# Performance work log

Hardware: AMD Instinct MI355X
Metric: run time of the kernel (lower is better)

## Reference

```python
import jax, jax.numpy as jnp
import numpy as np

B, S, DM = 2, 2048, 1024
H, KVH = 16, 4
DK = DM // H          # 64
KV_DIM = DK * KVH     # 256
REP = H // KVH        # 4


def setup_inputs() -> dict:
    key = jax.random.key(0)
    ks = jax.random.split(key, 8)
    return {
        "query": jax.random.normal(ks[0], (B, S, DM), jnp.float32),
        "key": jax.random.normal(ks[1], (B, S, DM), jnp.float32),
        "value": jax.random.normal(ks[2], (B, S, DM), jnp.float32),
        "Wq": jax.random.normal(ks[3], (DM, DM), jnp.float32) * 0.02,
        "bq": jnp.zeros((DM,), jnp.float32),
        "Wk": jax.random.normal(ks[4], (KV_DIM, DM), jnp.float32) * 0.02,
        "bk": jnp.zeros((KV_DIM,), jnp.float32),
        "Wv": jax.random.normal(ks[5], (KV_DIM, DM), jnp.float32) * 0.02,
        "bv": jnp.zeros((KV_DIM,), jnp.float32),
        "Wo": jax.random.normal(ks[6], (DM, DM), jnp.float32) * 0.02,
        "bo": jnp.zeros((DM,), jnp.float32),
    }


def reference(query, key, value, Wq, bq, Wk, bk, Wv, bv, Wo, bo):
    b, s, dm = query.shape
    # torch Linear: y = x @ W.T + b
    Q = (query @ Wq.T + bq).reshape(b, s, H, DK).transpose(0, 2, 1, 3)    # [b,H,s,dk]
    K = (key @ Wk.T + bk).reshape(b, s, KVH, DK).transpose(0, 2, 1, 3)    # [b,KVH,s,dk]
    V = (value @ Wv.T + bv).reshape(b, s, KVH, DK).transpose(0, 2, 1, 3)  # [b,KVH,s,dk]
    # group query heads by kv head instead of repeat_interleave-ing K/V
    Qg = Q.reshape(b, KVH, REP, s, DK)                                    # [b,g,r,s,dk]
    scale = 1.0 / np.sqrt(DK)
    scores = jnp.einsum('bgrqd,bgkd->bgrqk', Qg, K) * scale               # [b,g,r,s,s]
    attn = jax.nn.softmax(scores, axis=-1)
    ctx = jnp.einsum('bgrqk,bgkd->bgrqd', attn, V)                        # [b,g,r,s,dk]
    ctx = ctx.reshape(b, H, s, DK).transpose(0, 2, 1, 3).reshape(b, s, dm)
    out = ctx @ Wo.T + bo
    return out, attn.reshape(b, H, s, s)
```

## Files before the change

### kernel.cpp

```cpp
#include <hip/hip_runtime.h>

#define S_LEN 2048
#define DMODEL 1024
#define NH 16
#define NKVH 4
#define DKH 64
#define KVD 256
#define SCALE_LOG2E 0.18033688f

typedef __bf16 bf16;
typedef bf16  bf16x8 __attribute__((ext_vector_type(8)));
typedef bf16  bf16x4 __attribute__((ext_vector_type(4)));
typedef float f32x4  __attribute__((ext_vector_type(4)));
typedef bf16x8 bf16x8_a __attribute__((may_alias));
typedef bf16x4 bf16x4_a __attribute__((may_alias));
typedef float f32x4g __attribute__((ext_vector_type(4), may_alias));

#define VWAIT(N)                                             \
    do {                                                     \
        asm volatile("s_waitcnt vmcnt(" #N ")" ::: "memory");\
        __builtin_amdgcn_sched_barrier(0);                   \
    } while (0)

__device__ __forceinline__ void gll16(const bf16* g, bf16* l) {
    __builtin_amdgcn_global_load_lds(
        (const __attribute__((address_space(1))) void*)g,
        (__attribute__((address_space(3))) void*)l, 16, 0, 0);
}

__global__ __launch_bounds__(256) void cast3_bf16(const float* __restrict__ a,
                                                  const float* __restrict__ b,
                                                  const float* __restrict__ c,
                                                  bf16* __restrict__ oa, bf16* __restrict__ ob,
                                                  bf16* __restrict__ oc, int n4) {
    const float* src = blockIdx.y == 0 ? a : blockIdx.y == 1 ? b : c;
    bf16* dst = blockIdx.y == 0 ? oa : blockIdx.y == 1 ? ob : oc;
    int stride = gridDim.x * blockDim.x;
    for (int i = blockIdx.x * blockDim.x + threadIdx.x; i < n4; i += stride) {
        f32x4g v = ((const f32x4g*)src)[i];
        bf16x4 o;
        o[0] = (bf16)v[0]; o[1] = (bf16)v[1]; o[2] = (bf16)v[2]; o[3] = (bf16)v[3];
        ((bf16x4*)dst)[i] = o;
    }
}

__global__ __launch_bounds__(256) void cast4_bf16(const float* __restrict__ a,
                                                  const float* __restrict__ b,
                                                  const float* __restrict__ c,
                                                  const float* __restrict__ d,
                                                  bf16* __restrict__ oa, bf16* __restrict__ ob,
                                                  bf16* __restrict__ oc, bf16* __restrict__ od,
                                                  int n4big, int n4small) {
    const int y = blockIdx.y;
    const float* src = y == 0 ? a : y == 1 ? b : y == 2 ? c : d;
    bf16* dst = y == 0 ? oa : y == 1 ? ob : y == 2 ? oc : od;
    const int n4 = y < 2 ? n4big : n4small;
    int stride = gridDim.x * blockDim.x;
    for (int i = blockIdx.x * blockDim.x + threadIdx.x; i < n4; i += stride) {
        f32x4g v = ((const f32x4g*)src)[i];
        bf16x4 o;
        o[0] = (bf16)v[0]; o[1] = (bf16)v[1]; o[2] = (bf16)v[2]; o[3] = (bf16)v[3];
        ((bf16x4*)dst)[i] = o;
    }
}

template <int OUTF32>
__device__ __forceinline__ void gemm_body(const bf16* __restrict__ A,
                                          const bf16* __restrict__ Bw,
                                          const float* __restrict__ bias,
                                          void* __restrict__ Cout, int bm, int bn, int N,
                                          int K, bf16* As, bf16* Bs) {
    const int tid = threadIdx.x, wave = tid >> 6, lane = tid & 63;
    const int l15 = lane & 15, lhi = lane >> 4;
    const int wr = (wave >> 1) * 64, wc = (wave & 1) * 64;
    f32x4 acc[4][4] = {};
    const size_t arow0 = (size_t)bm * 128 * K;
    const size_t brow0 = (size_t)bn * 128 * K;

    for (int kt = 0; kt < K; kt += 32) {
#pragma unroll
        for (int i = 0; i < 2; ++i) {
            int base = i * 2048 + wave * 512;
            int flat = base + lane * 8;
            int r = flat >> 5, c = flat & 31;
            gll16(A + arow0 + (size_t)r * K + kt + c, &As[base]);
            gll16(Bw + brow0 + (size_t)r * K + kt + c, &Bs[base]);
        }
        __syncthreads();
        bf16x8 af[4], bfr[4];
#pragma unroll
        for (int mi = 0; mi < 4; ++mi)
            af[mi] = *(const bf16x8_a*)&As[(wr + mi * 16 + l15) * 32 + lhi * 8];
#pragma unroll
        for (int ni = 0; ni < 4; ++ni)
            bfr[ni] = *(const bf16x8_a*)&Bs[(wc + ni * 16 + l15) * 32 + lhi * 8];
#pragma unroll
        for (int mi = 0; mi < 4; ++mi)
#pragma unroll
            for (int ni = 0; ni < 4; ++ni)
                acc[mi][ni] = __builtin_amdgcn_mfma_f32_16x16x32_bf16(
                    af[mi], bfr[ni], acc[mi][ni], 0, 0, 0);
        __syncthreads();
    }
#pragma unroll
    for (int mi = 0; mi < 4; ++mi)
#pragma unroll
        for (int ni = 0; ni < 4; ++ni)
#pragma unroll
            for (int j = 0; j < 4; ++j) {
                int row = bm * 128 + wr + mi * 16 + lhi * 4 + j;
                int col = bn * 128 + wc + ni * 16 + l15;
                float v = acc[mi][ni][j] + bias[col];
                if (OUTF32)
                    ((float*)Cout)[(size_t)row * N + col] = v;
                else
                    ((bf16*)Cout)[(size_t)row * N + col] = (bf16)v;
            }
}

template <int OUTF32>
__global__ __launch_bounds__(256) void gemm_bt(const bf16* __restrict__ A,
                                               const bf16* __restrict__ Bw,
                                               const float* __restrict__ bias,
                                               void* __restrict__ Cout,
                                               int M, int N, int K) {
    __shared__ bf16 As[4096];
    __shared__ bf16 Bs[4096];
    gemm_body<OUTF32>(A, Bw, bias, Cout, blockIdx.x, blockIdx.y, N, K, As, Bs);
}

__global__ __launch_bounds__(256) void gemm_qkv(const bf16* __restrict__ qx,
                                                const bf16* __restrict__ kx,
                                                const bf16* __restrict__ vx,
                                                const bf16* __restrict__ wqx,
                                                const bf16* __restrict__ wkx,
                                                const bf16* __restrict__ wvx,
                                                const float* __restrict__ bq,
                                                const float* __restrict__ bk,
                                                const float* __restrict__ bv,
                                                bf16* __restrict__ Qp, bf16* __restrict__ Kp,
                                                bf16* __restrict__ Vp) {
    __shared__ bf16 As[4096];
    __shared__ bf16 Bs[4096];
    const int by = blockIdx.y;
    const bf16* A;
    const bf16* Bw;
    const float* bias;
    bf16* C;
    int N, bn;
    if (by < 8) {
        A = qx; Bw = wqx; bias = bq; C = Qp; N = 1024; bn = by;
    } else if (by < 10) {
        A = kx; Bw = wkx; bias = bk; C = Kp; N = 256; bn = by - 8;
    } else {
        A = vx; Bw = wvx; bias = bv; C = Vp; N = 256; bn = by - 10;
    }
    gemm_body<0>(A, Bw, bias, C, blockIdx.x, bn, N, 1024, As, Bs);
}

__global__ __launch_bounds__(256) void vtrans(const bf16* __restrict__ V,
                                              bf16* __restrict__ VT) {
    __shared__ bf16 t[64][65];
    const int s0 = blockIdx.x * 64;
    const int bg = blockIdx.y;
    const int b = bg >> 2, g = bg & 3;
#pragma unroll
    for (int i = 0; i < 16; ++i) {
        int flat = threadIdx.x + i * 256;
        int r = flat >> 6, c = flat & 63;
        t[c][r] = V[(size_t)(b * S_LEN + s0 + r) * KVD + g * DKH + c];
    }
    __syncthreads();
#pragma unroll
    for (int i = 0; i < 16; ++i) {
        int flat = threadIdx.x + i * 256;
        int d = flat >> 6, si = flat & 63;
        VT[((size_t)bg * DKH + d) * S_LEN + s0 + si] = t[d][si];
    }
}

__global__ __launch_bounds__(512, 4) void attn_all(const bf16* __restrict__ Qp,
                                                   const bf16* __restrict__ Kp,
                                                   const bf16* __restrict__ VT,
                                                   float* __restrict__ attn_out,
                                                   bf16* __restrict__ ctx) {
    __shared__ bf16 KV[4][4096];
    __shared__ bf16 Pw[8][1024];
    const int raw = blockIdx.x;
    const int wg = (raw & 7) * 64 + (raw >> 3);
    const int bh = wg >> 4;
    const int qt = wg & 15;
    const int h = bh & (NH - 1), b = bh >> 4, g = h >> 2;
    const int tid = threadIdx.x, wave = tid >> 6, lane = tid & 63;
    const int l15 = lane & 15, lhi = lane >> 4;
    const int qw = qt * 128 + wave * 16;
    const int sw = (l15 & 7) << 4;

    const bf16* qb = Qp + (size_t)(b * S_LEN + qw + l15) * DMODEL + h * DKH + lhi * 8;
    bf16x8 aq0 = *(const bf16x8_a*)qb;
    bf16x8 aq1 = *(const bf16x8_a*)(qb + 32);

    const int srow = tid >> 3;
    const int scc = (tid & 7) ^ (srow & 7);
    const bf16* ksrc = Kp + (size_t)(b * S_LEN + srow) * KVD + g * DKH + scc * 8;
    const bf16* vsrc = VT + ((size_t)(b * NKVH + g) * DKH + srow) * S_LEN + scc * 8;

    gll16(ksrc, &KV[0][wave * 512]);
    gll16(ksrc + (size_t)64 * KVD, &KV[1][wave * 512]);
    float lsum = 0.f;
    for (int c = 0; c < 32; ++c) {
        if (c < 30) gll16(ksrc + (size_t)((c + 2) * 64) * KVD, &KV[(c + 2) & 3][wave * 512]);
        if (c < 30) { VWAIT(2); } else if (c == 30) { VWAIT(1); } else { VWAIT(0); }
        __builtin_amdgcn_s_barrier();
        const char* kc = (const char*)&KV[c & 3][0];
        f32x4 a0 = {0.f, 0.f, 0.f, 0.f}, a1 = a0, a2 = a0, a3 = a0;
        __builtin_amdgcn_s_setprio(1);
        {
            const int rb = l15 * 128;
            bf16x8 k0 = *(const bf16x8_a*)(kc + rb + ((lhi * 16) ^ sw));
            bf16x8 k1 = *(const bf16x8_a*)(kc + rb + ((lhi * 16 + 64) ^ sw));
            a0 = __builtin_amdgcn_mfma_f32_16x16x32_bf16(k0, aq0, a0, 0, 0, 0);
            a0 = __builtin_amdgcn_mfma_f32_16x16x32_bf16(k1, aq1, a0, 0, 0, 0);
        }
        {
            const int rb = (16 + l15) * 128;
            bf16x8 k0 = *(const bf16x8_a*)(kc + rb + ((lhi * 16) ^ sw));
            bf16x8 k1 = *(const bf16x8_a*)(kc + rb + ((lhi * 16 + 64) ^ sw));
            a1 = __builtin_amdgcn_mfma_f32_16x16x32_bf16(k0, aq0, a1, 0, 0, 0);
            a1 = __builtin_amdgcn_mfma_f32_16x16x32_bf16(k1, aq1, a1, 0, 0, 0);
        }
        {
            const int rb = (32 + l15) * 128;
            bf16x8 k0 = *(const bf16x8_a*)(kc + rb + ((lhi * 16) ^ sw));
            bf16x8 k1 = *(const bf16x8_a*)(kc + rb + ((lhi * 16 + 64) ^ sw));
            a2 = __builtin_amdgcn_mfma_f32_16x16x32_bf16(k0, aq0, a2, 0, 0, 0);
            a2 = __builtin_amdgcn_mfma_f32_16x16x32_bf16(k1, aq1, a2, 0, 0, 0);
        }
        {
            const int rb = (48 + l15) * 128;
            bf16x8 k0 = *(const bf16x8_a*)(kc + rb + ((lhi * 16) ^ sw));
            bf16x8 k1 = *(const bf16x8_a*)(kc + rb + ((lhi * 16 + 64) ^ sw));
            a3 = __builtin_amdgcn_mfma_f32_16x16x32_bf16(k0, aq0, a3, 0, 0, 0);
            a3 = __builtin_amdgcn_mfma_f32_16x16x32_bf16(k1, aq1, a3, 0, 0, 0);
        }
        __builtin_amdgcn_s_setprio(0);
#pragma unroll
        for (int j = 0; j < 4; ++j)
            lsum += __builtin_exp2f(a0[j] * SCALE_LOG2E) + __builtin_exp2f(a1[j] * SCALE_LOG2E) +
                    __builtin_exp2f(a2[j] * SCALE_LOG2E) + __builtin_exp2f(a3[j] * SCALE_LOG2E);
    }
    lsum += __shfl_xor(lsum, 16, 64);
    lsum += __shfl_xor(lsum, 32, 64);
    const float nlog = -__builtin_log2f(lsum);

    gll16(ksrc, &KV[0][wave * 512]);
    gll16(vsrc, &KV[2][wave * 512]);

    f32x4 cacc[4] = {};
    char* pl = (char*)&Pw[wave][0] + l15 * 128;
    char* pls = (char*)&Pw[wave][0];
    const int stslot = lane & 15;
    const int strow4 = lane >> 4;
    float* gstb = attn_out + ((size_t)bh * S_LEN + qw) * S_LEN;

    for (int c = 0; c < 32; ++c) {
        if (c == 0) { VWAIT(0); } else { VWAIT(4); }
        __builtin_amdgcn_s_barrier();
        if (c < 31) {
            gll16(ksrc + (size_t)((c + 1) * 64) * KVD, &KV[(c + 1) & 1][wave * 512]);
            gll16(vsrc + (c + 1) * 64, &KV[2 + ((c + 1) & 1)][wave * 512]);
            __builtin_amdgcn_sched_barrier(0);
        }
        const char* kc = (const char*)&KV[c & 1][0];
        f32x4 a0 = {0.f, 0.f, 0.f, 0.f}, a1 = a0, a2 = a0, a3 = a0;
        __builtin_amdgcn_s_setprio(1);
        {
            const int rb = l15 * 128;
            bf16x8 k0 = *(const bf16x8_a*)(kc + rb + ((lhi * 16) ^ sw));
            bf16x8 k1 = *(const bf16x8_a*)(kc + rb + ((lhi * 16 + 64) ^ sw));
            a0 = __builtin_amdgcn_mfma_f32_16x16x32_bf16(k0, aq0, a0, 0, 0, 0);
            a0 = __builtin_amdgcn_mfma_f32_16x16x32_bf16(k1, aq1, a0, 0, 0, 0);
        }
        {
            const int rb = (16 + l15) * 128;
            bf16x8 k0 = *(const bf16x8_a*)(kc + rb + ((lhi * 16) ^ sw));
            bf16x8 k1 = *(const bf16x8_a*)(kc + rb + ((lhi * 16 + 64) ^ sw));
            a1 = __builtin_amdgcn_mfma_f32_16x16x32_bf16(k0, aq0, a1, 0, 0, 0);
            a1 = __builtin_amdgcn_mfma_f32_16x16x32_bf16(k1, aq1, a1, 0, 0, 0);
        }
        {
            const int rb = (32 + l15) * 128;
            bf16x8 k0 = *(const bf16x8_a*)(kc + rb + ((lhi * 16) ^ sw));
            bf16x8 k1 = *(const bf16x8_a*)(kc + rb + ((lhi * 16 + 64) ^ sw));
            a2 = __builtin_amdgcn_mfma_f32_16x16x32_bf16(k0, aq0, a2, 0, 0, 0);
            a2 = __builtin_amdgcn_mfma_f32_16x16x32_bf16(k1, aq1, a2, 0, 0, 0);
        }
        {
            const int rb = (48 + l15) * 128;
            bf16x8 k0 = *(const bf16x8_a*)(kc + rb + ((lhi * 16) ^ sw));
            bf16x8 k1 = *(const bf16x8_a*)(kc + rb + ((lhi * 16 + 64) ^ sw));
            a3 = __builtin_amdgcn_mfma_f32_16x16x32_bf16(k0, aq0, a3, 0, 0, 0);
            a3 = __builtin_amdgcn_mfma_f32_16x16x32_bf16(k1, aq1, a3, 0, 0, 0);
        }
        __builtin_amdgcn_s_setprio(0);
        {
            bf16x4 p0, p1, p2, p3;
#pragma unroll
            for (int j = 0; j < 4; ++j) {
                p0[j] = (bf16)__builtin_exp2f(__builtin_fmaf(a0[j], SCALE_LOG2E, nlog));
                p1[j] = (bf16)__builtin_exp2f(__builtin_fmaf(a1[j], SCALE_LOG2E, nlog));
                p2[j] = (bf16)__builtin_exp2f(__builtin_fmaf(a2[j], SCALE_LOG2E, nlog));
                p3[j] = (bf16)__builtin_exp2f(__builtin_fmaf(a3[j], SCALE_LOG2E, nlog));
            }
            *(bf16x4_a*)(pl + ((0 * 32 + lhi * 8) ^ sw)) = p0;
            *(bf16x4_a*)(pl + ((1 * 32 + lhi * 8) ^ sw)) = p1;
            *(bf16x4_a*)(pl + ((2 * 32 + lhi * 8) ^ sw)) = p2;
            *(bf16x4_a*)(pl + ((3 * 32 + lhi * 8) ^ sw)) = p3;
        }
        bf16x8 ap0 = *(const bf16x8_a*)(pl + ((lhi * 16) ^ sw));
        bf16x8 ap1 = *(const bf16x8_a*)(pl + ((lhi * 16 + 64) ^ sw));
        const char* vc = (const char*)&KV[2 + (c & 1)][0];
        __builtin_amdgcn_s_setprio(1);
#pragma unroll
        for (int t = 0; t < 4; ++t) {
            const int vb = (t * 16 + l15) * 128;
            bf16x8 v0 = *(const bf16x8_a*)(vc + vb + ((lhi * 16) ^ sw));
            bf16x8 v1 = *(const bf16x8_a*)(vc + vb + ((lhi * 16 + 64) ^ sw));
            cacc[t] = __builtin_amdgcn_mfma_f32_16x16x32_bf16(ap0, v0, cacc[t], 0, 0, 0);
            cacc[t] = __builtin_amdgcn_mfma_f32_16x16x32_bf16(ap1, v1, cacc[t], 0, 0, 0);
        }
        __builtin_amdgcn_s_setprio(0);
#pragma unroll
        for (int t = 0; t < 4; ++t) {
            const int r = t * 4 + strow4;
            bf16x4 pv4 =
                *(const bf16x4_a*)(pls + r * 128 + ((stslot * 8) ^ ((r & 7) << 4)));
            f32x4 pf4;
#pragma unroll
            for (int j = 0; j < 4; ++j) pf4[j] = (float)pv4[j];
            *(f32x4g*)(gstb + (size_t)r * S_LEN + c * 64 + stslot * 4) = pf4;
        }
    }
#pragma unroll
    for (int t = 0; t < 4; ++t)
#pragma unroll
        for (int j = 0; j < 4; ++j) {
            int row = qw + lhi * 4 + j;
            ctx[(size_t)(b * S_LEN + row) * DMODEL + h * DKH + t * 16 + l15] =
                (bf16)cacc[t][j];
        }
}

extern "C" void kernel_launch(void* const* d_in, const int* in_sizes, int n_in,
                              void* d_out, int out_size, void* d_ws, size_t ws_size,
                              hipStream_t stream) {
    const float* query = (const float*)d_in[0];
    const float* key_i = (const float*)d_in[1];
    const float* value = (const float*)d_in[2];
    const float* Wq = (const float*)d_in[3];
    const float* bq = (const float*)d_in[4];
    const float* Wk = (const float*)d_in[5];
    const float* bk = (const float*)d_in[6];
    const float* Wv = (const float*)d_in[7];
    const float* bv = (const float*)d_in[8];
    const float* Wo = (const float*)d_in[9];
    const float* bo = (const float*)d_in[10];

    char* ws = (char*)d_ws;
    bf16* qx = (bf16*)(ws + 0);
    bf16* kx = (bf16*)(ws + ((size_t)8 << 20));
    bf16* vx = (bf16*)(ws + ((size_t)16 << 20));
    bf16* wqx = (bf16*)(ws + ((size_t)32 << 20));
    bf16* wkx = (bf16*)(ws + ((size_t)34 << 20));
    bf16* wvx = (bf16*)(ws + ((size_t)34 << 20) + ((size_t)512 << 10));
    bf16* wox = (bf16*)(ws + ((size_t)35 << 20));
    bf16* Qp = (bf16*)(ws + ((size_t)37 << 20));
    bf16* Kp = (bf16*)(ws + ((size_t)45 << 20));
    bf16* Vp = (bf16*)(ws + ((size_t)47 << 20));
    bf16* VT = (bf16*)(ws + ((size_t)49 << 20));
    bf16* ctxb = (bf16*)(ws + ((size_t)51 << 20));

    const int BS = 2 * S_LEN;

    cast3_bf16<<<dim3(1024, 3), 256, 0, stream>>>(query, key_i, value, qx, kx, vx,
                                                  BS * DMODEL / 4);
    cast4_bf16<<<dim3(1024, 4), 256, 0, stream>>>(Wq, Wo, Wk, Wv, wqx, wox, wkx, wvx,
                                                  DMODEL * DMODEL / 4, KVD * DMODEL / 4);

    gemm_qkv<<<dim3(32, 12), 256, 0, stream>>>(qx, kx, vx, wqx, wkx, wvx, bq, bk, bv, Qp, Kp,
                                               Vp);

    vtrans<<<dim3(32, 8), 256, 0, stream>>>(Vp, VT);

    float* attn_out = (float*)d_out + (size_t)BS * DMODEL;
    attn_all<<<512, 512, 0, stream>>>(Qp, Kp, VT, attn_out, ctxb);

    gemm_bt<1><<<dim3(32, 8), 256, 0, stream>>>(ctxb, wox, bo, (float*)d_out, BS, DMODEL, DMODEL);
}
```

Measured before the change: 236.9 us.

## Merge cast kernels and restructure softmax-denominator pass into 128-key double-buffered chunks

Merges the two fp32-to-bf16 cast launches into a single seven-way launch, removing one kernel launch. In the attention kernel's first pass, which computes the row-sum of exponentials, the 4-deep 64-key prefetch ring becomes a 2-deep ring of 128-key chunks. This halves the number of barriers and interleaves the exp2 work with the MFMAs. Each iteration now waits for all outstanding loads before proceeding, which can expose load latency, and an extra barrier is added before the buffers are reused by the second pass.

```diff
diff --git a/kernel.cpp b/kernel.cpp
--- a/kernel.cpp
+++ b/kernel.cpp
@@ -28,33 +28,31 @@
         (__attribute__((address_space(3))) void*)l, 16, 0, 0);
 }
 
-__global__ __launch_bounds__(256) void cast3_bf16(const float* __restrict__ a,
-                                                  const float* __restrict__ b,
-                                                  const float* __restrict__ c,
-                                                  bf16* __restrict__ oa, bf16* __restrict__ ob,
-                                                  bf16* __restrict__ oc, int n4) {
-    const float* src = blockIdx.y == 0 ? a : blockIdx.y == 1 ? b : c;
-    bf16* dst = blockIdx.y == 0 ? oa : blockIdx.y == 1 ? ob : oc;
-    int stride = gridDim.x * blockDim.x;
-    for (int i = blockIdx.x * blockDim.x + threadIdx.x; i < n4; i += stride) {
-        f32x4g v = ((const f32x4g*)src)[i];
-        bf16x4 o;
-        o[0] = (bf16)v[0]; o[1] = (bf16)v[1]; o[2] = (bf16)v[2]; o[3] = (bf16)v[3];
-        ((bf16x4*)dst)[i] = o;
-    }
-}
-
-__global__ __launch_bounds__(256) void cast4_bf16(const float* __restrict__ a,
-                                                  const float* __restrict__ b,
-                                                  const float* __restrict__ c,
-                                                  const float* __restrict__ d,
-                                                  bf16* __restrict__ oa, bf16* __restrict__ ob,
-                                                  bf16* __restrict__ oc, bf16* __restrict__ od,
-                                                  int n4big, int n4small) {
+__global__ __launch_bounds__(256) void cast_all(const float* __restrict__ i0,
+                                                const float* __restrict__ i1,
+                                                const float* __restrict__ i2,
+                                                const float* __restrict__ i3,
+                                                const float* __restrict__ i4,
+                                                const float* __restrict__ i5,
+                                                const float* __restrict__ i6,
+                                                bf16* __restrict__ o0, bf16* __restrict__ o1,
+                                                bf16* __restrict__ o2, bf16* __restrict__ o3,
+                                                bf16* __restrict__ o4, bf16* __restrict__ o5,
+                                                bf16* __restrict__ o6, int nbig, int nmid,
+                                                int nsmall) {
     const int y = blockIdx.y;
-    const float* src = y == 0 ? a : y == 1 ? b : y == 2 ? c : d;
-    bf16* dst = y == 0 ? oa : y == 1 ? ob : y == 2 ? oc : od;
-    const int n4 = y < 2 ? n4big : n4small;
+    const float* src;
+    bf16* dst;
+    int n4;
+    switch (y) {
+        case 0: src = i0; dst = o0; n4 = nbig; break;
+        case 1: src = i1; dst = o1; n4 = nbig; break;
+        case 2: src = i2; dst = o2; n4 = nbig; break;
+        case 3: src = i3; dst = o3; n4 = nmid; break;
+        case 4: src = i4; dst = o4; n4 = nmid; break;
+        case 5: src = i5; dst = o5; n4 = nsmall; break;
+        default: src = i6; dst = o6; n4 = nsmall; break;
+    }
     int stride = gridDim.x * blockDim.x;
     for (int i = blockIdx.x * blockDim.x + threadIdx.x; i < n4; i += stride) {
         f32x4g v = ((const f32x4g*)src)[i];
@@ -208,51 +206,36 @@
     gll16(ksrc, &KV[0][wave * 512]);
     gll16(ksrc + (size_t)64 * KVD, &KV[1][wave * 512]);
     float lsum = 0.f;
-    for (int c = 0; c < 32; ++c) {
-        if (c < 30) gll16(ksrc + (size_t)((c + 2) * 64) * KVD, &KV[(c + 2) & 3][wave * 512]);
-        if (c < 30) { VWAIT(2); } else if (c == 30) { VWAIT(1); } else { VWAIT(0); }
+    for (int c = 0; c < 16; ++c) {
+        VWAIT(0);
         __builtin_amdgcn_s_barrier();
-        const char* kc = (const char*)&KV[c & 3][0];
-        f32x4 a0 = {0.f, 0.f, 0.f, 0.f}, a1 = a0, a2 = a0, a3 = a0;
+        if (c < 15) {
+            const bf16* s = ksrc + (size_t)((c + 1) * 128) * KVD;
+            gll16(s, &KV[((c + 1) & 1) * 2][wave * 512]);
+            gll16(s + (size_t)64 * KVD, &KV[((c + 1) & 1) * 2 + 1][wave * 512]);
+        }
+        const char* kcl = (const char*)&KV[(c & 1) * 2][0];
+        const char* kch = (const char*)&KV[(c & 1) * 2 + 1][0];
         __builtin_amdgcn_s_setprio(1);
-        {
-            const int rb = l15 * 128;
-            bf16x8 k0 = *(const bf16x8_a*)(kc + rb + ((lhi * 16) ^ sw));
-            bf16x8 k1 = *(const bf16x8_a*)(kc + rb + ((lhi * 16 + 64) ^ sw));
-            a0 = __builtin_amdgcn_mfma_f32_16x16x32_bf16(k0, aq0, a0, 0, 0, 0);
-            a0 = __builtin_amdgcn_mfma_f32_16x16x32_bf16(k1, aq1, a0, 0, 0, 0);
-        }
-        {
-            const int rb = (16 + l15) * 128;
-            bf16x8 k0 = *(const bf16x8_a*)(kc + rb + ((lhi * 16) ^ sw));
-            bf16x8 k1 = *(const bf16x8_a*)(kc + rb + ((lhi * 16 + 64) ^ sw));
-            a1 = __builtin_amdgcn_mfma_f32_16x16x32_bf16(k0, aq0, a1, 0, 0, 0);
-            a1 = __builtin_amdgcn_mfma_f32_16x16x32_bf16(k1, aq1, a1, 0, 0, 0);
-        }
-        {
-            const int rb = (32 + l15) * 128;
-            bf16x8 k0 = *(const bf16x8_a*)(kc + rb + ((lhi * 16) ^ sw));
-            bf16x8 k1 = *(const bf16x8_a*)(kc + rb + ((lhi * 16 + 64) ^ sw));
-            a2 = __builtin_amdgcn_mfma_f32_16x16x32_bf16(k0, aq0, a2, 0, 0, 0);
-            a2 = __builtin_amdgcn_mfma_f32_16x16x32_bf16(k1, aq1, a2, 0, 0, 0);
-        }
-        {
-            const int rb = (48 + l15) * 128;
-            bf16x8 k0 = *(const bf16x8_a*)(kc + rb + ((lhi * 16) ^ sw));
-            bf16x8 k1 = *(const bf16x8_a*)(kc + rb + ((lhi * 16 + 64) ^ sw));
-            a3 = __builtin_amdgcn_mfma_f32_16x16x32_bf16(k0, aq0, a3, 0, 0, 0);
-            a3 = __builtin_amdgcn_mfma_f32_16x16x32_bf16(k1, aq1, a3, 0, 0, 0);
+#pragma unroll
+        for (int s8 = 0; s8 < 8; ++s8) {
+            const char* base = s8 < 4 ? kcl : kch;
+            const int rb = ((s8 & 3) * 16 + l15) * 128;
+            bf16x8 k0 = *(const bf16x8_a*)(base + rb + ((lhi * 16) ^ sw));
+            bf16x8 k1 = *(const bf16x8_a*)(base + rb + ((lhi * 16 + 64) ^ sw));
+            f32x4 a = {0.f, 0.f, 0.f, 0.f};
+            a = __builtin_amdgcn_mfma_f32_16x16x32_bf16(k0, aq0, a, 0, 0, 0);
+            a = __builtin_amdgcn_mfma_f32_16x16x32_bf16(k1, aq1, a, 0, 0, 0);
+            lsum += __builtin_exp2f(a[0] * SCALE_LOG2E) + __builtin_exp2f(a[1] * SCALE_LOG2E) +
+                    __builtin_exp2f(a[2] * SCALE_LOG2E) + __builtin_exp2f(a[3] * SCALE_LOG2E);
         }
         __builtin_amdgcn_s_setprio(0);
-#pragma unroll
-        for (int j = 0; j < 4; ++j)
-            lsum += __builtin_exp2f(a0[j] * SCALE_LOG2E) + __builtin_exp2f(a1[j] * SCALE_LOG2E) +
-                    __builtin_exp2f(a2[j] * SCALE_LOG2E) + __builtin_exp2f(a3[j] * SCALE_LOG2E);
     }
     lsum += __shfl_xor(lsum, 16, 64);
     lsum += __shfl_xor(lsum, 32, 64);
     const float nlog = -__builtin_log2f(lsum);
 
+    __builtin_amdgcn_s_barrier();
     gll16(ksrc, &KV[0][wave * 512]);
     gll16(vsrc, &KV[2][wave * 512]);
 
@@ -382,10 +365,9 @@
 
     const int BS = 2 * S_LEN;
 
-    cast3_bf16<<<dim3(1024, 3), 256, 0, stream>>>(query, key_i, value, qx, kx, vx,
-                                                  BS * DMODEL / 4);
-    cast4_bf16<<<dim3(1024, 4), 256, 0, stream>>>(Wq, Wo, Wk, Wv, wqx, wox, wkx, wvx,
-                                                  DMODEL * DMODEL / 4, KVD * DMODEL / 4);
+    cast_all<<<dim3(1024, 7), 256, 0, stream>>>(query, key_i, value, Wq, Wo, Wk, Wv, qx, kx,
+                                                vx, wqx, wox, wkx, wvx, BS * DMODEL / 4,
+                                                DMODEL * DMODEL / 4, KVD * DMODEL / 4);
 
     gemm_qkv<<<dim3(32, 12), 256, 0, stream>>>(qx, kx, vx, wqx, wkx, wvx, bq, bk, bv, Qp, Kp,
                                                Vp);
```

Measured after the change: 242.7 us. 1.02x slower.
